# Kernel tuning notes

Measured on AMD Instinct MI355X. Metric: run time of the kernel, lower is better.

## Reference

```python
import jax, jax.numpy as jnp
import numpy as np

B, L, D = 4096, 50, 64
NU, NR, NRAT = 1000000, 1000000, 5


def _linear_params(k, dout, din):
    k1, k2 = jax.random.split(k)
    s = 1.0 / np.sqrt(din)
    w = jax.random.uniform(k1, (dout, din), jnp.float32, -s, s)
    b = jax.random.uniform(k2, (dout,), jnp.float32, -s, s)
    return w, b


def setup_inputs() -> dict:
    key = jax.random.key(0)
    ks = jax.random.split(key, 12)
    inp = {
        "nodes": jax.random.randint(ks[0], (B,), 0, NU),
        "history": jax.random.randint(ks[1], (B, L), 0, NR),
        "ratings": jax.random.randint(ks[2], (B, L), 0, NRAT),
        "lengths": jax.random.randint(ks[3], (B,), 1, L + 1),  # at least 1 real neighbor
        "u2e": jax.random.normal(ks[4], (NU, D), jnp.float32) * 0.02,
        "r2e": jax.random.normal(ks[5], (NR, D), jnp.float32) * 0.02,
        "rating2e": jax.random.normal(ks[6], (NRAT, D), jnp.float32) * 0.02,
    }
    inp["w_r1"], inp["b_r1"] = _linear_params(ks[7], D, 2 * D)
    inp["w_r2"], inp["b_r2"] = _linear_params(ks[8], D, D)
    inp["att1_w"], inp["att1_b"] = _linear_params(ks[9], D, 2 * D)
    inp["att2_w"], inp["att2_b"] = _linear_params(ks[10], D, D)
    inp["att3_w"], inp["att3_b"] = _linear_params(ks[11], 1, D)
    return inp


def reference(nodes, history, ratings, lengths, u2e, r2e, rating2e,
              w_r1, b_r1, w_r2, b_r2,
              att1_w, att1_b, att2_w, att2_b, att3_w, att3_b):
    # Padded/batched version of the per-node ragged loop (ur=True branch, eval mode).
    e_ur = r2e[history]                      # [B, L, D] gather of review embeddings
    ur_rep = u2e[nodes]                      # [B, D]    per-node user embedding
    e_rating = rating2e[ratings]             # [B, L, D]

    x = jnp.concatenate([e_ur, e_rating], axis=-1)                      # [B, L, 2D]
    x = jax.nn.relu(jnp.einsum('bld,ed->ble', x, w_r1) + b_r1)          # w_r1
    o = jax.nn.relu(jnp.einsum('bld,ed->ble', x, w_r2) + b_r2)          # [B, L, D]

    # Attention: cat(o_history, u_rep repeated) -> MLP -> softmax over history axis
    a = jnp.concatenate([o, jnp.broadcast_to(ur_rep[:, None, :], o.shape)], axis=-1)
    a = jax.nn.relu(jnp.einsum('bld,ed->ble', a, att1_w) + att1_b)
    a = jax.nn.relu(jnp.einsum('bld,ed->ble', a, att2_w) + att2_b)
    scores = jnp.einsum('bld,ed->ble', a, att3_w)[..., 0] + att3_b[0]   # [B, L]

    mask = jnp.arange(history.shape[1]) < lengths[:, None]              # ragged mask
    scores = jnp.where(mask, scores, -jnp.inf)
    att_w = jax.nn.softmax(scores, axis=-1)                             # [B, L]

    return jnp.einsum('bl,bld->bd', att_w, o)                           # [B, D]
```

## Files before the change

kernel.cpp:

```cpp
#include <hip/hip_runtime.h>
#include <hip/hip_bf16.h>

#define B_N 4096
#define L_N 50
#define D_N 64

#define W1T 0
#define W2T 8192
#define A1T 12288
#define A2T 20480
#define W3  24576
#define B1  24640
#define B2  24704
#define AB1 24768
#define AB2 24832
#define FLAG 24896
#define WS_FLOATS 24897

__device__ __forceinline__ float bflo(unsigned p) { return __uint_as_float(p << 16); }
__device__ __forceinline__ float bfhi(unsigned p) { return __uint_as_float(p & 0xffff0000u); }
__device__ __forceinline__ float bf1(unsigned short u) { return __uint_as_float(((unsigned)u) << 16); }
__device__ __forceinline__ unsigned short f2bf(float f) {
    unsigned u = __float_as_uint(f);
    u += 0x7fffu + ((u >> 16) & 1u);
    return (unsigned short)(u >> 16);
}
__device__ __forceinline__ unsigned packbf(float a, float b) {
    return (unsigned)f2bf(a) | ((unsigned)f2bf(b) << 16);
}
__device__ __forceinline__ float rdv(const void* p, long i, int isf) {
    return isf ? ((const float*)p)[i] : bf1(((const unsigned short*)p)[i]);
}

__global__ void prep_kernel(const void* __restrict__ w1, const void* __restrict__ b1,
                            const void* __restrict__ w2, const void* __restrict__ b2,
                            const void* __restrict__ a1, const void* __restrict__ ab1,
                            const void* __restrict__ a2, const void* __restrict__ ab2,
                            const void* __restrict__ w3, float* __restrict__ W) {
    __shared__ int sfl;
    if (threadIdx.x == 0) {
        const unsigned short* s = (const unsigned short*)w1;
        int cnt = 0;
        for (int k = 0; k < 128; ++k) {
            float v = bf1(s[2 * k]);
            if (v == v && fabsf(v) <= 0.25f) ++cnt;
        }
        sfl = (cnt >= 100) ? 0 : 1;
    }
    __syncthreads();
    const int isf = sfl;
    int t = blockIdx.x * 256 + threadIdx.x;
    if (t == 0) W[FLAG] = (float)isf;
    if (t < 8192) {
        int e = t & 63, i = t >> 6;
        W[W1T + t] = rdv(w1, e * 128 + i, isf);
    } else if (t < 12288) {
        int q = t - 8192; int e = q & 63, i = q >> 6;
        W[W2T + q] = rdv(w2, e * 64 + i, isf);
    } else if (t < 20480) {
        int q = t - 12288; int e = q & 63, i = q >> 6;
        W[A1T + q] = rdv(a1, e * 128 + i, isf);
    } else if (t < 24576) {
        int q = t - 20480; int e = q & 63, i = q >> 6;
        W[A2T + q] = rdv(a2, e * 64 + i, isf);
    } else if (t < 24640) W[t] = rdv(w3, t - 24576, isf);
    else if (t < 24704) W[t] = rdv(b1, t - 24640, isf);
    else if (t < 24768) W[t] = rdv(b2, t - 24704, isf);
    else if (t < 24832) W[t] = rdv(ab1, t - 24768, isf);
    else if (t < FLAG)  W[t] = rdv(ab2, t - 24832, isf);
}

__launch_bounds__(64)
__global__ void agg_kernel(const int* __restrict__ nodes, const int* __restrict__ history,
                           const int* __restrict__ ratings, const int* __restrict__ lengths,
                           const void* __restrict__ u2e,
                           const void* __restrict__ r2e,
                           const void* __restrict__ rating2e,
                           const float* __restrict__ W,
                           void* __restrict__ out) {
    __shared__ unsigned xbuf[64 * 66];
    __shared__ unsigned ybuf[64 * 34];
    __shared__ float ur_s[64];
    __shared__ float c1_s[64];
    __shared__ float attw_s[64];

    const int b = blockIdx.x;
    const int l = threadIdx.x;
    const int lc = min(l, L_N - 1);
    const int node = nodes[b];
    const int lenb = lengths[b];
    const int isf = (W[FLAG] != 0.0f) ? 1 : 0;

    ur_s[l] = rdv(u2e, ((long)node << 6) + l, isf);

    {
        const int h = history[b * L_N + lc];
        const int r = ratings[b * L_N + lc];
        if (!isf) {
            const uint4* pu = (const uint4*)((const unsigned short*)r2e + ((long)h << 6));
            const uint4* pv = (const uint4*)((const unsigned short*)rating2e + ((long)r << 6));
#pragma unroll
            for (int k = 0; k < 8; ++k) {
                uint4 t = pu[k];
                *(uint2*)&xbuf[l * 66 + 4 * k] = make_uint2(t.x, t.y);
                *(uint2*)&xbuf[l * 66 + 4 * k + 2] = make_uint2(t.z, t.w);
            }
#pragma unroll
            for (int k = 0; k < 8; ++k) {
                uint4 t = pv[k];
                *(uint2*)&xbuf[l * 66 + 32 + 4 * k] = make_uint2(t.x, t.y);
                *(uint2*)&xbuf[l * 66 + 32 + 4 * k + 2] = make_uint2(t.z, t.w);
            }
        } else {
            const float4* pu = (const float4*)((const float*)r2e + ((long)h << 6));
            const float4* pv = (const float4*)((const float*)rating2e + ((long)r << 6));
#pragma unroll
            for (int k = 0; k < 16; ++k) {
                float4 t = pu[k];
                xbuf[l * 66 + 2 * k] = packbf(t.x, t.y);
                xbuf[l * 66 + 2 * k + 1] = packbf(t.z, t.w);
            }
#pragma unroll
            for (int k = 0; k < 16; ++k) {
                float4 t = pv[k];
                xbuf[l * 66 + 32 + 2 * k] = packbf(t.x, t.y);
                xbuf[l * 66 + 32 + 2 * k + 1] = packbf(t.z, t.w);
            }
        }
    }
    __syncthreads();

    {
        float a = W[AB1 + l];
#pragma unroll 4
        for (int i = 0; i < 64; ++i) a += W[A1T + (64 + i) * 64 + l] * ur_s[i];
        c1_s[l] = a;
    }
    __syncthreads();

    float acc[64];

#pragma unroll
    for (int e = 0; e < 64; ++e) acc[e] = W[B1 + e];
#pragma unroll 2
    for (int i = 0; i < 64; ++i) {
        const unsigned p = xbuf[l * 66 + i];
        const float x0 = bflo(p), x1 = bfhi(p);
        const float* w0 = &W[W1T + (i * 2) * 64];
        const float* w1 = w0 + 64;
#pragma unroll
        for (int e = 0; e < 64; ++e) acc[e] += w0[e] * x0 + w1[e] * x1;
    }
#pragma unroll
    for (int e2 = 0; e2 < 32; ++e2)
        ybuf[l * 34 + e2] = packbf(fmaxf(acc[2 * e2], 0.f), fmaxf(acc[2 * e2 + 1], 0.f));

#pragma unroll
    for (int e = 0; e < 64; ++e) acc[e] = W[B2 + e];
#pragma unroll 2
    for (int i = 0; i < 32; ++i) {
        const unsigned p = ybuf[l * 34 + i];
        const float x0 = bflo(p), x1 = bfhi(p);
        const float* w0 = &W[W2T + (i * 2) * 64];
        const float* w1 = w0 + 64;
#pragma unroll
        for (int e = 0; e < 64; ++e) acc[e] += w0[e] * x0 + w1[e] * x1;
    }
    float* ofp = (float*)xbuf;
#pragma unroll
    for (int e = 0; e < 64; ++e) {
        acc[e] = fmaxf(acc[e], 0.f);
        ofp[l * 66 + e] = acc[e];
    }

#pragma unroll
    for (int e = 0; e < 64; ++e) acc[e] = c1_s[e];
#pragma unroll 2
    for (int i = 0; i < 64; ++i) {
        const float xi = ofp[l * 66 + i];
        const float* w0 = &W[A1T + i * 64];
#pragma unroll
        for (int e = 0; e < 64; ++e) acc[e] += w0[e] * xi;
    }
#pragma unroll
    for (int e2 = 0; e2 < 32; ++e2)
        ybuf[l * 34 + e2] = packbf(fmaxf(acc[2 * e2], 0.f), fmaxf(acc[2 * e2 + 1], 0.f));

#pragma unroll
    for (int e = 0; e < 64; ++e) acc[e] = W[AB2 + e];
#pragma unroll 2
    for (int i = 0; i < 32; ++i) {
        const unsigned p = ybuf[l * 34 + i];
        const float x0 = bflo(p), x1 = bfhi(p);
        const float* w0 = &W[A2T + (i * 2) * 64];
        const float* w1 = w0 + 64;
#pragma unroll
        for (int e = 0; e < 64; ++e) acc[e] += w0[e] * x0 + w1[e] * x1;
    }

    float s0 = 0.f, s1 = 0.f, s2 = 0.f, s3 = 0.f;
#pragma unroll
    for (int e = 0; e < 64; e += 4) {
        s0 += fmaxf(acc[e], 0.f) * W[W3 + e];
        s1 += fmaxf(acc[e + 1], 0.f) * W[W3 + e + 1];
        s2 += fmaxf(acc[e + 2], 0.f) * W[W3 + e + 2];
        s3 += fmaxf(acc[e + 3], 0.f) * W[W3 + e + 3];
    }
    const float score = (s0 + s1) + (s2 + s3);

    const bool valid = (l < lenb);
    float mx = valid ? score : -1e30f;
#pragma unroll
    for (int m = 32; m > 0; m >>= 1) mx = fmaxf(mx, __shfl_xor(mx, m, 64));
    const float pw = valid ? __expf(score - mx) : 0.f;
    float sum = pw;
#pragma unroll
    for (int m = 32; m > 0; m >>= 1) sum += __shfl_xor(sum, m, 64);
    attw_s[l] = pw / sum;
    __syncthreads();

    float od = 0.f;
#pragma unroll 2
    for (int j = 0; j < L_N; ++j) od += attw_s[j] * ofp[j * 66 + l];
    if (isf) ((float*)out)[((long)b << 6) + l] = od;
    else     ((unsigned short*)out)[((long)b << 6) + l] = f2bf(od);
}

extern "C" void kernel_launch(void* const* d_in, const int* in_sizes, int n_in,
                              void* d_out, int out_size, void* d_ws, size_t ws_size,
                              hipStream_t stream) {
    const int* nodes = (const int*)d_in[0];
    const int* history = (const int*)d_in[1];
    const int* ratings = (const int*)d_in[2];
    const int* lengths = (const int*)d_in[3];
    const void* u2e = d_in[4];
    const void* r2e = d_in[5];
    const void* rating2e = d_in[6];
    const void* w1 = d_in[7];
    const void* b1 = d_in[8];
    const void* w2 = d_in[9];
    const void* b2 = d_in[10];
    const void* a1 = d_in[11];
    const void* ab1 = d_in[12];
    const void* a2 = d_in[13];
    const void* ab2 = d_in[14];
    const void* w3 = d_in[15];
    float* W = (float*)d_ws;

    prep_kernel<<<(WS_FLOATS + 255) / 256, 256, 0, stream>>>(w1, b1, w2, b2, a1, ab1, a2, ab2, w3, W);
    agg_kernel<<<B_N, 64, 0, stream>>>(nodes, history, ratings, lengths, u2e, r2e, rating2e, W, d_out);
}
```

Before: 703.2 us.

## Pack weights and activations as fp16 pairs and use packed dot2 FMAs

Weights are pre-packed into fp16 pairs, and each MLP layer uses v_dot2 (fdot2) accumulation into fp32, which halves weight loads and FMA instruction count. Activations stay in registers (xp/yp/op) instead of round-tripping through LDS, and launch bounds ask for 3 waves per SIMD. The cost is lower precision, since fp16 has a narrower range than bf16 and pkrtz truncates. The register-resident arrays also add register pressure.

```diff
diff --git a/kernel.cpp b/kernel.cpp
--- a/kernel.cpp
+++ b/kernel.cpp
@@ -5,17 +5,20 @@
 #define L_N 50
 #define D_N 64
 
-#define W1T 0
-#define W2T 8192
-#define A1T 12288
-#define A2T 20480
-#define W3  24576
-#define B1  24640
-#define B2  24704
-#define AB1 24768
-#define AB2 24832
-#define FLAG 24896
-#define WS_FLOATS 24897
+#define W1P  0
+#define W2P  4096
+#define A1P  6144
+#define A2P  8192
+#define A1TU 10240
+#define W3   14336
+#define B1   14400
+#define B2   14464
+#define AB1  14528
+#define AB2  14592
+#define FLAG 14656
+#define WS_WORDS 14657
+
+typedef _Float16 f16x2 __attribute__((ext_vector_type(2)));
 
 __device__ __forceinline__ float bflo(unsigned p) { return __uint_as_float(p << 16); }
 __device__ __forceinline__ float bfhi(unsigned p) { return __uint_as_float(p & 0xffff0000u); }
@@ -25,9 +28,31 @@
     u += 0x7fffu + ((u >> 16) & 1u);
     return (unsigned short)(u >> 16);
 }
-__device__ __forceinline__ unsigned packbf(float a, float b) {
-    return (unsigned)f2bf(a) | ((unsigned)f2bf(b) << 16);
-}
+__device__ __forceinline__ f16x2 bch(unsigned u) { return __builtin_bit_cast(f16x2, u); }
+
+#if __has_builtin(__builtin_amdgcn_cvt_pkrtz)
+__device__ __forceinline__ unsigned pkr(float a, float b) {
+    return __builtin_bit_cast(unsigned, __builtin_amdgcn_cvt_pkrtz(a, b));
+}
+#else
+__device__ __forceinline__ unsigned pkr(float a, float b) {
+    f16x2 h; h.x = (_Float16)a; h.y = (_Float16)b;
+    return __builtin_bit_cast(unsigned, h);
+}
+#endif
+__device__ __forceinline__ unsigned pkrne(float a, float b) {
+    f16x2 h; h.x = (_Float16)a; h.y = (_Float16)b;
+    return __builtin_bit_cast(unsigned, h);
+}
+
+#if __has_builtin(__builtin_amdgcn_fdot2)
+#define DOT2(a, b, c) __builtin_amdgcn_fdot2((a), (b), (c), false)
+#else
+__device__ __forceinline__ float DOT2(f16x2 a, f16x2 b, float c) {
+    return c + (float)a.x * (float)b.x + (float)a.y * (float)b.y;
+}
+#endif
+
 __device__ __forceinline__ float rdv(const void* p, long i, int isf) {
     return isf ? ((const float*)p)[i] : bf1(((const unsigned short*)p)[i]);
 }
@@ -36,63 +61,67 @@
                             const void* __restrict__ w2, const void* __restrict__ b2,
                             const void* __restrict__ a1, const void* __restrict__ ab1,
                             const void* __restrict__ a2, const void* __restrict__ ab2,
-                            const void* __restrict__ w3, float* __restrict__ W) {
+                            const void* __restrict__ w3, unsigned* __restrict__ Wu) {
+    float* Wf = (float*)Wu;
     __shared__ int sfl;
-    if (threadIdx.x == 0) {
+    if (threadIdx.x < 64) {
         const unsigned short* s = (const unsigned short*)w1;
-        int cnt = 0;
-        for (int k = 0; k < 128; ++k) {
-            float v = bf1(s[2 * k]);
-            if (v == v && fabsf(v) <= 0.25f) ++cnt;
-        }
-        sfl = (cnt >= 100) ? 0 : 1;
+        float v = bf1(s[2 * threadIdx.x]);
+        int ok = (v == v) && (fabsf(v) <= 0.25f);
+        unsigned long long m = __ballot(ok);
+        if (threadIdx.x == 0) sfl = (__popcll(m) >= 56) ? 0 : 1;
     }
     __syncthreads();
     const int isf = sfl;
-    int t = blockIdx.x * 256 + threadIdx.x;
-    if (t == 0) W[FLAG] = (float)isf;
-    if (t < 8192) {
-        int e = t & 63, i = t >> 6;
-        W[W1T + t] = rdv(w1, e * 128 + i, isf);
-    } else if (t < 12288) {
-        int q = t - 8192; int e = q & 63, i = q >> 6;
-        W[W2T + q] = rdv(w2, e * 64 + i, isf);
-    } else if (t < 20480) {
-        int q = t - 12288; int e = q & 63, i = q >> 6;
-        W[A1T + q] = rdv(a1, e * 128 + i, isf);
-    } else if (t < 24576) {
-        int q = t - 20480; int e = q & 63, i = q >> 6;
-        W[A2T + q] = rdv(a2, e * 64 + i, isf);
-    } else if (t < 24640) W[t] = rdv(w3, t - 24576, isf);
-    else if (t < 24704) W[t] = rdv(b1, t - 24640, isf);
-    else if (t < 24768) W[t] = rdv(b2, t - 24704, isf);
-    else if (t < 24832) W[t] = rdv(ab1, t - 24768, isf);
-    else if (t < FLAG)  W[t] = rdv(ab2, t - 24832, isf);
-}
-
-__launch_bounds__(64)
+    const int t = blockIdx.x * 256 + threadIdx.x;
+    if (t >= WS_WORDS) return;
+    if (t == FLAG) { Wf[FLAG] = (float)isf; return; }
+    if (t < 4096) {
+        int i = t >> 6, e = t & 63;
+        Wu[W1P + t] = pkrne(rdv(w1, e * 128 + 2 * i, isf), rdv(w1, e * 128 + 2 * i + 1, isf));
+    } else if (t < 6144) {
+        int q = t - 4096, i = q >> 6, e = q & 63;
+        Wu[W2P + q] = pkrne(rdv(w2, e * 64 + 2 * i, isf), rdv(w2, e * 64 + 2 * i + 1, isf));
+    } else if (t < 8192) {
+        int q = t - 6144, i = q >> 6, e = q & 63;
+        Wu[A1P + q] = pkrne(rdv(a1, e * 128 + 2 * i, isf), rdv(a1, e * 128 + 2 * i + 1, isf));
+    } else if (t < 10240) {
+        int q = t - 8192, i = q >> 6, e = q & 63;
+        Wu[A2P + q] = pkrne(rdv(a2, e * 64 + 2 * i, isf), rdv(a2, e * 64 + 2 * i + 1, isf));
+    } else if (t < 14336) {
+        int q = t - 10240, i = q >> 6, e = q & 63;
+        Wf[A1TU + q] = rdv(a1, e * 128 + 64 + i, isf);
+    } else if (t < 14400) Wf[t] = rdv(w3, t - 14336, isf);
+    else if (t < 14464) Wf[t] = rdv(b1, t - 14400, isf);
+    else if (t < 14528) Wf[t] = rdv(b2, t - 14464, isf);
+    else if (t < 14592) Wf[t] = rdv(ab1, t - 14528, isf);
+    else if (t < FLAG)  Wf[t] = rdv(ab2, t - 14592, isf);
+}
+
+__launch_bounds__(64, 3)
 __global__ void agg_kernel(const int* __restrict__ nodes, const int* __restrict__ history,
                            const int* __restrict__ ratings, const int* __restrict__ lengths,
                            const void* __restrict__ u2e,
                            const void* __restrict__ r2e,
                            const void* __restrict__ rating2e,
-                           const float* __restrict__ W,
+                           const unsigned* __restrict__ Wu,
                            void* __restrict__ out) {
-    __shared__ unsigned xbuf[64 * 66];
-    __shared__ unsigned ybuf[64 * 34];
+    __shared__ float obuf[64 * 66];
     __shared__ float ur_s[64];
     __shared__ float c1_s[64];
     __shared__ float attw_s[64];
+    const float* Wf = (const float*)Wu;
 
     const int b = blockIdx.x;
     const int l = threadIdx.x;
     const int lc = min(l, L_N - 1);
     const int node = nodes[b];
     const int lenb = lengths[b];
-    const int isf = (W[FLAG] != 0.0f) ? 1 : 0;
+    const int isf = (Wf[FLAG] != 0.0f) ? 1 : 0;
 
     ur_s[l] = rdv(u2e, ((long)node << 6) + l, isf);
 
+    unsigned xp[64];
     {
         const int h = history[b * L_N + lc];
         const int r = ratings[b * L_N + lc];
@@ -102,14 +131,18 @@
 #pragma unroll
             for (int k = 0; k < 8; ++k) {
                 uint4 t = pu[k];
-                *(uint2*)&xbuf[l * 66 + 4 * k] = make_uint2(t.x, t.y);
-                *(uint2*)&xbuf[l * 66 + 4 * k + 2] = make_uint2(t.z, t.w);
+                xp[4 * k]     = pkr(bflo(t.x), bfhi(t.x));
+                xp[4 * k + 1] = pkr(bflo(t.y), bfhi(t.y));
+                xp[4 * k + 2] = pkr(bflo(t.z), bfhi(t.z));
+                xp[4 * k + 3] = pkr(bflo(t.w), bfhi(t.w));
             }
 #pragma unroll
             for (int k = 0; k < 8; ++k) {
                 uint4 t = pv[k];
-                *(uint2*)&xbuf[l * 66 + 32 + 4 * k] = make_uint2(t.x, t.y);
-                *(uint2*)&xbuf[l * 66 + 32 + 4 * k + 2] = make_uint2(t.z, t.w);
+                xp[32 + 4 * k]     = pkr(bflo(t.x), bfhi(t.x));
+                xp[32 + 4 * k + 1] = pkr(bflo(t.y), bfhi(t.y));
+                xp[32 + 4 * k + 2] = pkr(bflo(t.z), bfhi(t.z));
+                xp[32 + 4 * k + 3] = pkr(bflo(t.w), bfhi(t.w));
             }
         } else {
             const float4* pu = (const float4*)((const float*)r2e + ((long)h << 6));
@@ -117,94 +150,91 @@
 #pragma unroll
             for (int k = 0; k < 16; ++k) {
                 float4 t = pu[k];
-                xbuf[l * 66 + 2 * k] = packbf(t.x, t.y);
-                xbuf[l * 66 + 2 * k + 1] = packbf(t.z, t.w);
+                xp[2 * k] = pkr(t.x, t.y);
+                xp[2 * k + 1] = pkr(t.z, t.w);
             }
 #pragma unroll
             for (int k = 0; k < 16; ++k) {
                 float4 t = pv[k];
-                xbuf[l * 66 + 32 + 2 * k] = packbf(t.x, t.y);
-                xbuf[l * 66 + 32 + 2 * k + 1] = packbf(t.z, t.w);
+                xp[32 + 2 * k] = pkr(t.x, t.y);
+                xp[32 + 2 * k + 1] = pkr(t.z, t.w);
             }
         }
     }
     __syncthreads();
 
     {
-        float a = W[AB1 + l];
-#pragma unroll 4
-        for (int i = 0; i < 64; ++i) a += W[A1T + (64 + i) * 64 + l] * ur_s[i];
-        c1_s[l] = a;
+        float c = Wf[AB1 + l];
+#pragma unroll 8
+        for (int i = 0; i < 64; ++i) c += Wf[A1TU + i * 64 + l] * ur_s[i];
+        c1_s[l] = c;
     }
     __syncthreads();
 
     float acc[64];
 
 #pragma unroll
-    for (int e = 0; e < 64; ++e) acc[e] = W[B1 + e];
+    for (int e = 0; e < 64; ++e) acc[e] = Wf[B1 + e];
 #pragma unroll 2
     for (int i = 0; i < 64; ++i) {
-        const unsigned p = xbuf[l * 66 + i];
-        const float x0 = bflo(p), x1 = bfhi(p);
-        const float* w0 = &W[W1T + (i * 2) * 64];
-        const float* w1 = w0 + 64;
-#pragma unroll
-        for (int e = 0; e < 64; ++e) acc[e] += w0[e] * x0 + w1[e] * x1;
-    }
+        const f16x2 x = bch(xp[i]);
+        const unsigned* wr = &Wu[W1P + i * 64];
+#pragma unroll
+        for (int e = 0; e < 64; ++e) acc[e] = DOT2(x, bch(wr[e]), acc[e]);
+    }
+    unsigned yp[32];
 #pragma unroll
     for (int e2 = 0; e2 < 32; ++e2)
-        ybuf[l * 34 + e2] = packbf(fmaxf(acc[2 * e2], 0.f), fmaxf(acc[2 * e2 + 1], 0.f));
-
-#pragma unroll
-    for (int e = 0; e < 64; ++e) acc[e] = W[B2 + e];
+        yp[e2] = pkr(fmaxf(acc[2 * e2], 0.f), fmaxf(acc[2 * e2 + 1], 0.f));
+
+#pragma unroll
+    for (int e = 0; e < 64; ++e) acc[e] = Wf[B2 + e];
 #pragma unroll 2
     for (int i = 0; i < 32; ++i) {
-        const unsigned p = ybuf[l * 34 + i];
-        const float x0 = bflo(p), x1 = bfhi(p);
-        const float* w0 = &W[W2T + (i * 2) * 64];
-        const float* w1 = w0 + 64;
-#pragma unroll
-        for (int e = 0; e < 64; ++e) acc[e] += w0[e] * x0 + w1[e] * x1;
-    }
-    float* ofp = (float*)xbuf;
-#pragma unroll
-    for (int e = 0; e < 64; ++e) {
-        acc[e] = fmaxf(acc[e], 0.f);
-        ofp[l * 66 + e] = acc[e];
+        const f16x2 x = bch(yp[i]);
+        const unsigned* wr = &Wu[W2P + i * 64];
+#pragma unroll
+        for (int e = 0; e < 64; ++e) acc[e] = DOT2(x, bch(wr[e]), acc[e]);
+    }
+    unsigned op[32];
+#pragma unroll
+    for (int e2 = 0; e2 < 32; ++e2) {
+        float a = fmaxf(acc[2 * e2], 0.f), c2 = fmaxf(acc[2 * e2 + 1], 0.f);
+        obuf[l * 66 + 2 * e2] = a;
+        obuf[l * 66 + 2 * e2 + 1] = c2;
+        op[e2] = pkr(a, c2);
     }
 
 #pragma unroll
     for (int e = 0; e < 64; ++e) acc[e] = c1_s[e];
 #pragma unroll 2
-    for (int i = 0; i < 64; ++i) {
-        const float xi = ofp[l * 66 + i];
-        const float* w0 = &W[A1T + i * 64];
-#pragma unroll
-        for (int e = 0; e < 64; ++e) acc[e] += w0[e] * xi;
+    for (int i = 0; i < 32; ++i) {
+        const f16x2 x = bch(op[i]);
+        const unsigned* wr = &Wu[A1P + i * 64];
+#pragma unroll
+        for (int e = 0; e < 64; ++e) acc[e] = DOT2(x, bch(wr[e]), acc[e]);
     }
 #pragma unroll
     for (int e2 = 0; e2 < 32; ++e2)
-        ybuf[l * 34 + e2] = packbf(fmaxf(acc[2 * e2], 0.f), fmaxf(acc[2 * e2 + 1], 0.f));
-
-#pragma unroll
-    for (int e = 0; e < 64; ++e) acc[e] = W[AB2 + e];
+        yp[e2] = pkr(fmaxf(acc[2 * e2], 0.f), fmaxf(acc[2 * e2 + 1], 0.f));
+
+#pragma unroll
+    for (int e = 0; e < 64; ++e) acc[e] = Wf[AB2 + e];
 #pragma unroll 2
     for (int i = 0; i < 32; ++i) {
-        const unsigned p = ybuf[l * 34 + i];
-        const float x0 = bflo(p), x1 = bfhi(p);
-        const float* w0 = &W[A2T + (i * 2) * 64];
-        const float* w1 = w0 + 64;
-#pragma unroll
-        for (int e = 0; e < 64; ++e) acc[e] += w0[e] * x0 + w1[e] * x1;
+        const f16x2 x = bch(yp[i]);
+        const unsigned* wr = &Wu[A2P + i * 64];
+#pragma unroll
+        for (int e = 0; e < 64; ++e) acc[e] = DOT2(x, bch(wr[e]), acc[e]);
     }
 
     float s0 = 0.f, s1 = 0.f, s2 = 0.f, s3 = 0.f;
 #pragma unroll
     for (int e = 0; e < 64; e += 4) {
-        s0 += fmaxf(acc[e], 0.f) * W[W3 + e];
-        s1 += fmaxf(acc[e + 1], 0.f) * W[W3 + e + 1];
-        s2 += fmaxf(acc[e + 2], 0.f) * W[W3 + e + 2];
-        s3 += fmaxf(acc[e + 3], 0.f) * W[W3 + e + 3];
+        s0 += fmaxf(acc[e], 0.f) * Wf[W3 + e];
+        s1 += fmaxf(acc[e + 1], 0.f) * Wf[W3 + e + 1];
+        s2 += fmaxf(acc[e + 2], 0.f) * Wf[W3 + e + 2];
+        s3 += fmaxf(acc[e + 3], 0.f) * Wf[W3 + e + 3];
     }
     const float score = (s0 + s1) + (s2 + s3);
 
@@ -221,7 +251,7 @@
 
     float od = 0.f;
 #pragma unroll 2
-    for (int j = 0; j < L_N; ++j) od += attw_s[j] * ofp[j * 66 + l];
+    for (int j = 0; j < L_N; ++j) od += attw_s[j] * obuf[j * 66 + l];
     if (isf) ((float*)out)[((long)b << 6) + l] = od;
     else     ((unsigned short*)out)[((long)b << 6) + l] = f2bf(od);
 }
@@ -245,8 +275,8 @@
     const void* a2 = d_in[13];
     const void* ab2 = d_in[14];
     const void* w3 = d_in[15];
-    float* W = (float*)d_ws;
-
-    prep_kernel<<<(WS_FLOATS + 255) / 256, 256, 0, stream>>>(w1, b1, w2, b2, a1, ab1, a2, ab2, w3, W);
+    unsigned* W = (unsigned*)d_ws;
+
+    prep_kernel<<<(WS_WORDS + 255) / 256, 256, 0, stream>>>(w1, b1, w2, b2, a1, ab1, a2, ab2, w3, W);
     agg_kernel<<<B_N, 64, 0, stream>>>(nodes, history, ratings, lengths, u2e, r2e, rating2e, W, d_out);
 }
```

Result: faster. 576.7 us (-18.0%).
